# Performance work log

Measured on AMD Instinct MI355X. Metric: run time of the kernel, lower is better.

## Reference

```python
import jax, jax.numpy as jnp
import numpy as np

NUM_CLASSES = 7
B = 14336
D = 512
H_KDE = 0.2          # sklearn KernelDensity(bandwidth=0.2, kernel='gaussian')
KERNEL_MUL = 2.0
KERNEL_NUM = 5
BN_EPS = 1e-5


def _pairwise_sqdist(a, b):
    # ||a_i - b_j||^2 via gram trick; avoids the [n,n,d] broadcast tensor the torch code builds
    an = jnp.sum(a * a, axis=-1)
    bn = jnp.sum(b * b, axis=-1)
    d2 = an[:, None] + bn[None, :] - 2.0 * (a @ b.T)
    return jnp.maximum(d2, 0.0)


def _multi_kernel(total):
    # sum of KERNEL_NUM Gaussian kernels, bandwidths 1.25 * 2^i (bandwidth=5 / 2^(5//2))
    d2 = _pairwise_sqdist(total, total)
    bw0 = 5.0 / (KERNEL_MUL ** (KERNEL_NUM // 2))
    k = jnp.zeros_like(d2)
    for i in range(KERNEL_NUM):  # small fixed loop, avoids [5,n,n] intermediate
        k = k + jnp.exp(-d2 / (bw0 * (KERNEL_MUL ** i)))
    return k


def _mmd(src, tgt):
    m = src.shape[0]
    k = _multi_kernel(jnp.concatenate([src, tgt], axis=0))
    return jnp.mean(k[:m, :m] + k[m:, m:] - k[:m, m:] - k[m:, :m])


def _kde_weight(class_feats):
    # sklearn gaussian KDE: log p(x_i) = logsumexp_j(-||x_i-x_j||^2 / (2 h^2)) - log m - (d/2) log(2 pi h^2)
    # volume v = sum_i 1 / log p(x_i); weight = 1 / (v + 1e-5)
    C, m, d = class_feats.shape
    log_norm = -0.5 * d * jnp.log(2.0 * jnp.pi * (H_KDE ** 2)) - jnp.log(jnp.float32(m))

    def one(f):
        d2 = _pairwise_sqdist(f, f)
        logp = jax.nn.logsumexp(-d2 / (2.0 * (H_KDE ** 2)), axis=1) + log_norm
        return jnp.sum(1.0 / logp)

    v = jax.vmap(one)(class_feats)
    return 1.0 / (v + 1e-5)


def setup_inputs() -> dict:
    key = jax.random.key(0)
    k1, k2 = jax.random.split(key)
    fea = jax.random.normal(k1, (B, D), dtype=jnp.float32) * 0.05
    W_fc = jax.random.normal(k2, (NUM_CLASSES, D), dtype=jnp.float32) * 0.02
    gamma = jnp.ones((NUM_CLASSES,), dtype=jnp.float32)
    beta = jnp.zeros((NUM_CLASSES,), dtype=jnp.float32)
    # balanced, contiguous class blocks so per-class splits are static reshapes
    targets = jnp.repeat(jnp.arange(NUM_CLASSES, dtype=jnp.int32), B // NUM_CLASSES)
    return {"fea": fea, "W_fc": W_fc, "gamma": gamma, "beta": beta, "targets": targets}


def reference(fea, W_fc, gamma, beta, targets):
    Bn, d = fea.shape
    C = NUM_CLASSES
    m = Bn // C

    # out = BatchNorm1d(fc(fea)) in train mode (biased batch stats)
    logits = fea @ W_fc.T                              # [B, C]
    mu = jnp.mean(logits, axis=0)
    var = jnp.var(logits, axis=0)
    out = gamma * (logits - mu) / jnp.sqrt(var + BN_EPS) + beta

    # split_feature_makeLD with balanced contiguous targets -> static reshape
    cf = fea.reshape(C, m, d)                          # [C, m, D]

    # KDE density weights: computed on detached numpy features in the original -> stop_gradient
    w = jax.lax.stop_gradient(_kde_weight(cf))         # [C]

    def per_class(i):
        src = cf[i]
        # remove_element concatenates classes 0..i-1, i+1..C-1 in order;
        # first m rows of that = class 0 (class 1 when i == 0)
        tgt = cf[jnp.where(i > 0, 0, 1)]
        return _mmd(src, tgt)

    losses = jax.vmap(per_class)(jnp.arange(C))        # [C]
    affinity_loss = -jnp.sum(losses * w)
    return (out, affinity_loss)
```

## Files before the change

### kernel.cpp

```cpp
#include <hip/hip_runtime.h>

#define B_ROWS 14336
#define D_DIM  512
#define C_CLS  7
#define M_CLS  2048

typedef __attribute__((ext_vector_type(4))) float f32x4;

#define FP8_SCALE 64.0f
#define INV_2S2   (2.0f / 4096.0f)

typedef const __attribute__((address_space(1))) char gchar_t;
typedef __attribute__((address_space(3))) char lchar_t;

__device__ __forceinline__ void gload16(const char* g, char* l) {
  __builtin_amdgcn_global_load_lds((gchar_t*)g, (lchar_t*)l, 16, 0, 0);
}

__global__ __launch_bounds__(256) void k_prep(const float* __restrict__ fea,
                                              const float* __restrict__ W,
                                              char* __restrict__ f8p,
                                              float* __restrict__ an,
                                              float* __restrict__ logits,
                                              float* __restrict__ zb) {
  int t = threadIdx.x, wave = t >> 6, lane = t & 63;
  if (blockIdx.x == 0 && t < 64) zb[t] = 0.f;
  __shared__ char lrow[16 * 528];

  int r0 = blockIdx.x * 16;
#pragma unroll
  for (int k = 0; k < 4; ++k) {
    int rl = wave * 4 + k;
    int row = r0 + rl;
    const float4* fr4 = (const float4*)(fea + (size_t)row * D_DIM);
    float4 v0 = fr4[lane * 2], v1 = fr4[lane * 2 + 1];

    float p[8];
#pragma unroll
    for (int c = 0; c < 7; ++c) {
      const float4* w4 = (const float4*)(W + c * D_DIM);
      float4 q0 = w4[lane * 2], q1 = w4[lane * 2 + 1];
      p[c] = v0.x * q0.x + v0.y * q0.y + v0.z * q0.z + v0.w * q0.w +
             v1.x * q1.x + v1.y * q1.y + v1.z * q1.z + v1.w * q1.w;
    }
    p[7] = v0.x * v0.x + v0.y * v0.y + v0.z * v0.z + v0.w * v0.w +
           v1.x * v1.x + v1.y * v1.y + v1.z * v1.z + v1.w * v1.w;

#pragma unroll
    for (int c = 0; c < 8; ++c) {
      p[c] += __shfl_xor(p[c], 1);
      p[c] += __shfl_xor(p[c], 2);
      p[c] += __shfl_xor(p[c], 4);
    }
    int v = lane & 7;
    float y = p[0];
    y = (v == 1) ? p[1] : y;
    y = (v == 2) ? p[2] : y;
    y = (v == 3) ? p[3] : y;
    y = (v == 4) ? p[4] : y;
    y = (v == 5) ? p[5] : y;
    y = (v == 6) ? p[6] : y;
    y = (v == 7) ? p[7] : y;
    y += __shfl_xor(y, 8);
    y += __shfl_xor(y, 16);
    y += __shfl_xor(y, 32);
    if (lane < 7) logits[row * 7 + lane] = y;
    else if (lane == 7) an[row] = y;

    int w0 = __builtin_amdgcn_cvt_pk_fp8_f32(v0.x * FP8_SCALE, v0.y * FP8_SCALE, 0, 0);
    w0     = __builtin_amdgcn_cvt_pk_fp8_f32(v0.z * FP8_SCALE, v0.w * FP8_SCALE, w0, 1);
    int w1 = __builtin_amdgcn_cvt_pk_fp8_f32(v1.x * FP8_SCALE, v1.y * FP8_SCALE, 0, 0);
    w1     = __builtin_amdgcn_cvt_pk_fp8_f32(v1.z * FP8_SCALE, v1.w * FP8_SCALE, w1, 1);
    *(int2*)&lrow[rl * 528 + lane * 8] = make_int2(w0, w1);
  }
  __syncthreads();
  int4* outp = (int4*)f8p + (size_t)blockIdx.x * 512;
#pragma unroll
  for (int pi = 0; pi < 2; ++pi) {
    int idx = pi * 256 + t;
    int kp = idx >> 6, l = idx & 63;
    int sr = l & 15, qk = l >> 4;
    int2 lo = *(const int2*)&lrow[sr * 528 + kp * 64 + qk * 8];
    int2 hi = *(const int2*)&lrow[sr * 528 + kp * 64 + 32 + qk * 8];
    outp[idx] = make_int4(lo.x, lo.y, hi.x, hi.y);
  }
}

__global__ __launch_bounds__(512, 2) void k_gram(const char* __restrict__ f8p,
                                                 const float* __restrict__ an,
                                                 const float* __restrict__ logits,
                                                 float* __restrict__ S,
                                                 float* __restrict__ rs_part,
                                                 float* __restrict__ S1,
                                                 float* __restrict__ S2,
                                                 float* __restrict__ aff) {
  int b = blockIdx.x;
  int t = threadIdx.x, lane = t & 63, wave = t >> 6;
  if (b == 0 && t == 0) aff[0] = 0.f;

  if (b >= 636) {
    int idx = (b - 636) * 8 + wave;
    int c = idx >> 3, seg = idx & 7;
    int r0 = seg * 1792;
    float s1 = 0.f, s2 = 0.f;
    for (int j = lane; j < 1792; j += 64) {
      float v = logits[(size_t)(r0 + j) * 7 + c];
      s1 += v;
      s2 += v * v;
    }
#pragma unroll
    for (int o = 1; o < 64; o <<= 1) {
      s1 += __shfl_xor(s1, o);
      s2 += __shfl_xor(s2, o);
    }
    if (lane == 0) { atomicAdd(&S1[c], s1); atomicAdd(&S2[c], s2); }
    return;
  }

  __shared__ char ldsA[2][16384];
  __shared__ char ldsB[2][16384];
  __shared__ float bacc[8];

  int cls1, cls2, ti, tj, Sidx;
  bool self;
  if (b < 252) {
    int cls = b / 36, t36 = b - cls * 36;
    int a = 0, r = t36;
    while (r > a) { r -= a + 1; ++a; }
    ti = a; tj = r;
    cls1 = cls; cls2 = cls; Sidx = cls; self = true;
  } else {
    int e = b - 252;
    int p = e >> 6, t64 = e & 63;
    ti = t64 >> 3; tj = t64 & 7;
    cls1 = p + 1; cls2 = 0; Sidx = 7 + p; self = false;
  }
  int R0 = cls1 * 2048 + ti * 256;
  int C0 = cls2 * 2048 + tj * 256;

  const char* gA0 = f8p + ((size_t)(R0 >> 4) + wave * 2)     * 8192 + lane * 16;
  const char* gA1 = f8p + ((size_t)(R0 >> 4) + wave * 2 + 1) * 8192 + lane * 16;
  const char* gB0 = f8p + ((size_t)(C0 >> 4) + wave * 2)     * 8192 + lane * 16;
  const char* gB1 = f8p + ((size_t)(C0 >> 4) + wave * 2 + 1) * 8192 + lane * 16;

#define STAGE(kt_, bf_)                                                      \
  do {                                                                       \
    gload16(gA0 + (kt_) * 1024, &ldsA[bf_][(wave * 2) * 1024 + lane * 16]);  \
    gload16(gA1 + (kt_) * 1024, &ldsA[bf_][(wave * 2 + 1) * 1024 + lane * 16]); \
    gload16(gB0 + (kt_) * 1024, &ldsB[bf_][(wave * 2) * 1024 + lane * 16]);  \
    gload16(gB1 + (kt_) * 1024, &ldsB[bf_][(wave * 2 + 1) * 1024 + lane * 16]); \
  } while (0)

  int wr = wave >> 2, wc = wave & 3;
  int q = lane >> 4, s = lane & 15;

  f32x4 acc[8][4];
#pragma unroll
  for (int i = 0; i < 8; ++i)
#pragma unroll
    for (int j = 0; j < 4; ++j)
      acc[i][j] = (f32x4){0.f, 0.f, 0.f, 0.f};

  STAGE(0, 0);
  __syncthreads();

#pragma unroll 1
  for (int kt = 0; kt < 8; ++kt) {
    int cur = kt & 1;
    if (kt < 7) STAGE(kt + 1, cur ^ 1);
    const char* LA = &ldsA[cur][(wr * 8) * 1024 + lane * 16];
    const char* LB = &ldsB[cur][(wc * 4) * 1024 + lane * 16];
    longlong2 a_[8], bb_[4];
#pragma unroll
    for (int i = 0; i < 8; ++i) a_[i] = *(const longlong2*)(LA + i * 1024);
#pragma unroll
    for (int j = 0; j < 4; ++j) bb_[j] = *(const longlong2*)(LB + j * 1024);
    __builtin_amdgcn_s_setprio(1);
#pragma unroll
    for (int i = 0; i < 8; ++i)
#pragma unroll
      for (int j = 0; j < 4; ++j)
        acc[i][j] = __builtin_amdgcn_mfma_f32_16x16x32_fp8_fp8(
            a_[i].x, bb_[j].x, acc[i][j], 0, 0, 0);
#pragma unroll
    for (int i = 0; i < 8; ++i)
#pragma unroll
      for (int j = 0; j < 4; ++j)
        acc[i][j] = __builtin_amdgcn_mfma_f32_16x16x32_fp8_fp8(
            a_[i].y, bb_[j].y, acc[i][j], 0, 0, 0);
    __builtin_amdgcn_s_setprio(0);
    __syncthreads();
  }
#undef STAGE

  bool dg = self && (ti == tj);
  bool mirror = self && (ti > tj);
  float blockAcc = 0.f;
  float colAcc[4] = {0.f, 0.f, 0.f, 0.f};
  float anB_[4];
#pragma unroll
  for (int j = 0; j < 4; ++j) anB_[j] = an[C0 + wc * 64 + j * 16 + s];

#pragma unroll
  for (int i = 0; i < 8; ++i) {
    f32x4 anA_ = *(const f32x4*)&an[R0 + wr * 128 + i * 16 + q * 4];
#pragma unroll
    for (int rg = 0; rg < 4; ++rg) {
      int rl = wr * 128 + i * 16 + q * 4 + rg;
      float aA = anA_[rg];
      float rowAcc = 0.f;
#pragma unroll
      for (int j = 0; j < 4; ++j) {
        int cl = wc * 64 + j * 16 + s;
        float g = acc[i][j][rg];
        float d2 = fmaxf(aA + anB_[j] - g * INV_2S2, 0.f);
        if (dg && rl == cl) d2 = 0.f;
        float e1 = __expf(-0.05f * d2);
        float e2 = e1 * e1, e4 = e2 * e2, e8 = e4 * e4, e16 = e8 * e8;
        blockAcc += e1 + e2 + e4 + e8 + e16;
        if (self) {
          float ek = __expf(-12.5f * d2);
          rowAcc += ek;
          if (mirror) colAcc[j] += ek;
        }
      }
      if (self) {
        rowAcc += __shfl_xor(rowAcc, 1);
        rowAcc += __shfl_xor(rowAcc, 2);
        rowAcc += __shfl_xor(rowAcc, 4);
        rowAcc += __shfl_xor(rowAcc, 8);
        if (s == 0)
          rs_part[(size_t)(R0 + rl) * 48 + tj * 4 + wc] = rowAcc;
      }
    }
  }
  if (mirror) {
#pragma unroll
    for (int j = 0; j < 4; ++j) {
      float v = colAcc[j];
      v += __shfl_xor(v, 16);
      v += __shfl_xor(v, 32);
      if (q == 0)
        rs_part[(size_t)(C0 + wc * 64 + j * 16 + s) * 48 + 32 + ti * 2 + wr] = v;
    }
    blockAcc *= 2.f;
  }
#pragma unroll
  for (int o = 1; o < 64; o <<= 1) blockAcc += __shfl_xor(blockAcc, o);
  if (lane == 0) bacc[wave] = blockAcc;
  __syncthreads();
  if (t == 0) {
    float sB = 0.f;
#pragma unroll
    for (int w = 0; w < 8; ++w) sB += bacc[w];
    atomicAdd(&S[Sidx], sB);
  }
}

__global__ __launch_bounds__(1024) void k_final(const float* __restrict__ logits,
                                                const float* __restrict__ S1,
                                                const float* __restrict__ S2,
                                                const float* __restrict__ gamma,
                                                const float* __restrict__ beta,
                                                const float* __restrict__ rs_part,
                                                const float* __restrict__ S,
                                                float* __restrict__ out) {
  int b = blockIdx.x, t = threadIdx.x;
  if (b < 98) {
    int idx = b * 1024 + t;
    int row = idx / 7;
    int c = idx - row * 7;
    float mu = S1[c] * (1.f / 14336.f);
    float var = S2[c] * (1.f / 14336.f) - mu * mu;
    out[idx] = gamma[c] * (logits[idx] - mu) * rsqrtf(var + 1e-5f) + beta[c];
    return;
  }
  int c = b - 98;
  const float LOG_NORM = 345.9110632f;
  float v = 0.f;
  for (int i = t; i < M_CLS; i += 1024) {
    int bi = i >> 8;
    const float* rp = rs_part + (size_t)(c * M_CLS + i) * 48;
    float rsum = 0.f;
    int nd = 4 * bi + 4;
    for (int k = 0; k < nd; ++k) rsum += rp[k];
    for (int k = 34 + 2 * bi; k < 48; ++k) rsum += rp[k];
    v += 1.f / (logf(rsum) + LOG_NORM);
  }
#pragma unroll
  for (int o = 1; o < 64; o <<= 1) v += __shfl_xor(v, o);
  __shared__ float r[16];
  if ((t & 63) == 0) r[t >> 6] = v;
  __syncthreads();
  if (t == 0) {
    float vs = 0.f;
#pragma unroll
    for (int w = 0; w < 16; ++w) vs += r[w];
    float w = 1.f / (vs + 1e-5f);
    const float inv_m2 = 1.0f / ((float)M_CLS * (float)M_CLS);
    float Ssrc = S[c];
    float Stgt = (c > 0) ? S[0] : S[1];
    float X    = (c > 0) ? S[6 + c] : S[7];
    float mmd = (Ssrc + Stgt - 2.f * X) * inv_m2;
    atomicAdd(&out[100352], -mmd * w);
  }
}

extern "C" void kernel_launch(void* const* d_in, const int* in_sizes, int n_in,
                              void* d_out, int out_size, void* d_ws, size_t ws_size,
                              hipStream_t stream) {
  const float* fea   = (const float*)d_in[0];
  const float* W_fc  = (const float*)d_in[1];
  const float* gamma = (const float*)d_in[2];
  const float* beta  = (const float*)d_in[3];
  float* out = (float*)d_out;

  char* ws = (char*)d_ws;
  char* f8p = ws;
  float* fbase   = (float*)(ws + 7340032);
  float* an      = fbase;
  float* logits  = fbase + 14336;
  float* zb      = fbase + 114688;
  float* S1      = zb;
  float* S2      = zb + 7;
  float* S       = zb + 16;
  float* rs_part = fbase + 114752;

  k_prep <<<896, 256, 0, stream>>>(fea, W_fc, f8p, an, logits, zb);
  k_gram <<<643, 512, 0, stream>>>(f8p, an, logits, S, rs_part, S1, S2,
                                   out + 100352);
  k_final<<<105, 1024, 0, stream>>>(logits, S1, S2, gamma, beta, rs_part, S, out);
}
```

Before: 195.4 us.

## Remap gram blocks by XCD and overlap next-tile prefetch with explicit waitcnts

The block index is split so that blockIdx&7 picks a class. Consecutive blocks, which land on different XCDs, each work on one class, so that class's features stay in one XCD's L2. The cross-class tiles and the BN-stat reduction blocks are spread over the remaining slots, and the grid grows to 648. The K loop drops __syncthreads after issuing the prefetch and uses explicit vmcnt/lgkmcnt waits with raw barriers, so the next tile's global->LDS loads stay in flight during the MFMAs. The hand-placed waits rely on the exact count of outstanding loads being correct.

```diff
diff --git a/kernel.cpp b/kernel.cpp
--- a/kernel.cpp
+++ b/kernel.cpp
@@ -94,13 +94,13 @@
                                                  float* __restrict__ S1,
                                                  float* __restrict__ S2,
                                                  float* __restrict__ aff) {
-  int b = blockIdx.x;
+  int x = blockIdx.x & 7, u = blockIdx.x >> 3;
   int t = threadIdx.x, lane = t & 63, wave = t >> 6;
-  if (b == 0 && t == 0) aff[0] = 0.f;
-
-  if (b >= 636) {
-    int idx = (b - 636) * 8 + wave;
-    int c = idx >> 3, seg = idx & 7;
+  if (blockIdx.x == 0 && t == 0) aff[0] = 0.f;
+
+  if (u == 80) {
+    if (x >= 7) return;
+    int c = x, seg = wave;
     int r0 = seg * 1792;
     float s1 = 0.f, s2 = 0.f;
     for (int j = lane; j < 1792; j += 64) {
@@ -117,24 +117,26 @@
     return;
   }
 
+  int cls1, cls2, ti, tj, Sidx;
+  bool self;
+  if (x < 7 && u < 36) {
+    int a = 0, r = u;
+    while (r > a) { r -= a + 1; ++a; }
+    ti = a; tj = r;
+    cls1 = x; cls2 = x; Sidx = x; self = true;
+  } else {
+    int j;
+    if (x < 7) j = x * 44 + (u - 36);
+    else { if (u >= 76) return; j = 308 + u; }
+    int p = j >> 6, t64 = j & 63;
+    ti = t64 >> 3; tj = t64 & 7;
+    cls1 = p + 1; cls2 = 0; Sidx = 7 + p; self = false;
+  }
+
   __shared__ char ldsA[2][16384];
   __shared__ char ldsB[2][16384];
   __shared__ float bacc[8];
 
-  int cls1, cls2, ti, tj, Sidx;
-  bool self;
-  if (b < 252) {
-    int cls = b / 36, t36 = b - cls * 36;
-    int a = 0, r = t36;
-    while (r > a) { r -= a + 1; ++a; }
-    ti = a; tj = r;
-    cls1 = cls; cls2 = cls; Sidx = cls; self = true;
-  } else {
-    int e = b - 252;
-    int p = e >> 6, t64 = e & 63;
-    ti = t64 >> 3; tj = t64 & 7;
-    cls1 = p + 1; cls2 = 0; Sidx = 7 + p; self = false;
-  }
   int R0 = cls1 * 2048 + ti * 256;
   int C0 = cls2 * 2048 + tj * 256;
 
@@ -167,7 +169,14 @@
 #pragma unroll 1
   for (int kt = 0; kt < 8; ++kt) {
     int cur = kt & 1;
-    if (kt < 7) STAGE(kt + 1, cur ^ 1);
+    if (kt < 7) {
+      STAGE(kt + 1, cur ^ 1);
+      asm volatile("s_waitcnt vmcnt(4)" ::: "memory");
+    } else {
+      asm volatile("s_waitcnt vmcnt(0)" ::: "memory");
+    }
+    __builtin_amdgcn_s_barrier();
+    asm volatile("" ::: "memory");
     const char* LA = &ldsA[cur][(wr * 8) * 1024 + lane * 16];
     const char* LB = &ldsB[cur][(wc * 4) * 1024 + lane * 16];
     longlong2 a_[8], bb_[4];
@@ -175,6 +184,8 @@
     for (int i = 0; i < 8; ++i) a_[i] = *(const longlong2*)(LA + i * 1024);
 #pragma unroll
     for (int j = 0; j < 4; ++j) bb_[j] = *(const longlong2*)(LB + j * 1024);
+    asm volatile("s_waitcnt lgkmcnt(0)" ::: "memory");
+    __builtin_amdgcn_sched_barrier(0);
     __builtin_amdgcn_s_setprio(1);
 #pragma unroll
     for (int i = 0; i < 8; ++i)
@@ -189,7 +200,8 @@
         acc[i][j] = __builtin_amdgcn_mfma_f32_16x16x32_fp8_fp8(
             a_[i].y, bb_[j].y, acc[i][j], 0, 0, 0);
     __builtin_amdgcn_s_setprio(0);
-    __syncthreads();
+    __builtin_amdgcn_s_barrier();
+    asm volatile("" ::: "memory");
   }
 #undef STAGE
 
@@ -327,7 +339,7 @@
   float* rs_part = fbase + 114752;
 
   k_prep <<<896, 256, 0, stream>>>(fea, W_fc, f8p, an, logits, zb);
-  k_gram <<<643, 512, 0, stream>>>(f8p, an, logits, S, rs_part, S1, S2,
+  k_gram <<<648, 512, 0, stream>>>(f8p, an, logits, S, rs_part, S1, S2,
                                    out + 100352);
   k_final<<<105, 1024, 0, stream>>>(logits, S1, S2, gamma, beta, rs_part, S, out);
 }
```

Result: no change. 196.0 us (+0.3%).
